# Kernel optimization log

Measured on AMD Instinct MI355X. Metric: run time of the kernel, lower is better.

## Reference

```python
import jax, jax.numpy as jnp
import numpy as np
from jax import lax

CIN, COUT, K_EXP, KSZ = 128, 256, 8, 3
HIDDEN = CIN // 4  # reduction=4
B, H, W = 32, 56, 56
TEMP = 1.0


def setup_inputs() -> dict:
    key = jax.random.key(0)
    ks = jax.random.split(key, 6)
    x = jax.random.normal(ks[0], (B, CIN, H, W), dtype=jnp.float32)
    weight_bank = jax.random.normal(ks[1], (K_EXP, COUT, CIN, KSZ, KSZ), dtype=jnp.float32) * 0.02
    fc1_w = jax.random.normal(ks[2], (HIDDEN, CIN), dtype=jnp.float32) * (1.0 / np.sqrt(CIN))
    fc1_b = jnp.zeros((HIDDEN,), dtype=jnp.float32)
    fc2_w = jax.random.normal(ks[3], (K_EXP, HIDDEN), dtype=jnp.float32) * (1.0 / np.sqrt(HIDDEN))
    fc2_b = jnp.zeros((K_EXP,), dtype=jnp.float32)
    return {"x": x, "weight_bank": weight_bank, "fc1_w": fc1_w, "fc1_b": fc1_b,
            "fc2_w": fc2_w, "fc2_b": fc2_b}


def reference(x, weight_bank, fc1_w, fc1_b, fc2_w, fc2_b):
    b, cin, h, w = x.shape
    # Routing: GAP -> fc1 -> relu -> fc2 -> softmax(/T)
    v = jnp.mean(x, axis=(2, 3))                       # (B, cin)
    hdd = jax.nn.relu(v @ fc1_w.T + fc1_b)             # (B, hidden)
    logits = hdd @ fc2_w.T + fc2_b                     # (B, K)
    a = jax.nn.softmax(logits / TEMP, axis=1)          # (B, K)
    # Per-sample dynamic weights: (B, cout, cin, k, k)
    Wdyn = jnp.einsum('bk,kocij->bocij', a, weight_bank)
    # Batched per-sample conv via grouped convolution:
    # x -> (1, B*cin, H, W), Wdyn -> (B*cout, cin, k, k), groups=B
    xg = x.reshape(1, b * cin, h, w)
    wg = Wdyn.reshape(b * weight_bank.shape[1], cin, KSZ, KSZ)
    y = lax.conv_general_dilated(
        xg, wg,
        window_strides=(1, 1),
        padding=[(1, 1), (1, 1)],
        feature_group_count=b,
        dimension_numbers=('NCHW', 'OIHW', 'NCHW'),
    )
    return y.reshape(b, weight_bank.shape[1], y.shape[2], y.shape[3])
```

## Files before the change

kernel.cpp:

```cpp
#include <hip/hip_runtime.h>


#define CIN    128
#define COUT   256
#define KEXP   8
#define HIDDEN 32
#define B_     32
#define H_     56
#define W_     56
#define HW     3136
#define HP     58
#define WP     58
#define KK     1152

typedef float  v4f  __attribute__((ext_vector_type(4)));
typedef float  v16f __attribute__((ext_vector_type(16)));
typedef __bf16 v8bf __attribute__((ext_vector_type(8)));

__device__ __forceinline__ unsigned short f2bf(float x) {
  unsigned int u = __float_as_uint(x);
  u += 0x7fff + ((u >> 16) & 1);
  return (unsigned short)(u >> 16);
}

__device__ __forceinline__ void gl_lds16(const void* g, void* lds) {
  __builtin_amdgcn_global_load_lds(
      (__attribute__((address_space(1))) void*)(unsigned long long)(g),
      (__attribute__((address_space(3))) void*)(lds),
      16, 0, 0);
}

__global__ __launch_bounds__(256) void k_xpose(const float* __restrict__ x,
                                               unsigned short* __restrict__ xpt,
                                               float* __restrict__ gpart) {
  const int h = blockIdx.x, b = blockIdx.y, tid = threadIdx.x;
  __shared__ __align__(16) unsigned short tfb[56 * 132];
  __shared__ float gp[256];
  const float4* xr4 = (const float4*)x + (size_t)b * CIN * 784;

#pragma unroll
  for (int it = 0; it < 7; ++it) {
    int idx = it * 256 + tid;
    int c  = idx / 14;
    int wq = idx - c * 14;
    float4 q = xr4[(size_t)c * 784 + h * 14 + wq];
    int w0 = wq * 4;
    tfb[(w0 + 0) * 132 + c] = f2bf(q.x);
    tfb[(w0 + 1) * 132 + c] = f2bf(q.y);
    tfb[(w0 + 2) * 132 + c] = f2bf(q.z);
    tfb[(w0 + 3) * 132 + c] = f2bf(q.w);
  }
  __syncthreads();

  {
    int c = tid & 127, half = tid >> 7;
    float s = 0.f;
#pragma unroll
    for (int w = half * 28; w < half * 28 + 28; ++w)
      s += __uint_as_float((unsigned)tfb[w * 132 + c] << 16);
    gp[tid] = s;
  }

#pragma unroll
  for (int it = 0; it < 7; ++it) {
    int idx = it * 256 + tid;
    int w  = idx >> 5;
    int c4 = (idx & 31) << 2;
    ushort4 o = *(const ushort4*)(tfb + w * 132 + c4);
    *(ushort4*)(xpt + ((size_t)(b * HP + (h + 1)) * WP + (w + 1)) * CIN + c4) = o;
  }

  if (tid < 128) {
    size_t rb = (size_t)(b * HP + (h + 1)) * WP * CIN;
    xpt[rb + tid] = 0;
    xpt[rb + 57 * CIN + tid] = 0;
  }
  if (h == 0 || h == 55) {
    int hr = (h == 0) ? 0 : 57;
    size_t rb = (size_t)(b * HP + hr) * WP * CIN;
    ushort4 z; z.x = z.y = z.z = z.w = 0;
    for (int i = tid; i < 1856; i += 256)
      *(ushort4*)(xpt + rb + i * 4) = z;
  }

  __syncthreads();
  if (tid < 128)
    gpart[((size_t)h * B_ + b) * CIN + tid] =
        (gp[tid] + gp[tid + 128]) * (1.0f / 3136.0f);
}

__global__ void k_mlp(const float* __restrict__ gpart, const float* __restrict__ fc1w,
                      const float* __restrict__ fc1b, const float* __restrict__ fc2w,
                      const float* __restrict__ fc2b, float* __restrict__ aout) {
  const int b = blockIdx.x, t = threadIdx.x;
  __shared__ float vS[CIN];
  __shared__ float hid[HIDDEN];
  __shared__ float lg[KEXP];
  {
    float s = 0.f;
    for (int h = 0; h < H_; ++h) s += gpart[((size_t)h * B_ + b) * CIN + t];
    vS[t] = s;
  }
  __syncthreads();
  if (t < HIDDEN) {
    float s = fc1b[t];
    const float* wr = fc1w + t * CIN;
    for (int c = 0; c < CIN; ++c) s += vS[c] * wr[c];
    hid[t] = fmaxf(s, 0.f);
  }
  __syncthreads();
  if (t < KEXP) {
    float s = fc2b[t];
    const float* wr = fc2w + t * HIDDEN;
    for (int j = 0; j < HIDDEN; ++j) s += hid[j] * wr[j];
    lg[t] = s;
  }
  __syncthreads();
  if (t == 0) {
    float m = lg[0];
    for (int k = 1; k < KEXP; ++k) m = fmaxf(m, lg[k]);
    float e[KEXP], den = 0.f;
    for (int k = 0; k < KEXP; ++k) { e[k] = expf(lg[k] - m); den += e[k]; }
    float inv = 1.0f / den;
    for (int k = 0; k < KEXP; ++k) aout[b * KEXP + k] = e[k] * inv;
  }
}

__global__ __launch_bounds__(512) void k_wdyn(const float* __restrict__ aout,
                                              const float* __restrict__ bank,
                                              unsigned short* __restrict__ wdyn) {
  const int cout = blockIdx.x, tid = threadIdx.x;
  __shared__ float4 bS4[KEXP * 288];
  __shared__ float aS[B_ * KEXP];

  for (int idx = tid; idx < KEXP * 288; idx += 512) {
    int k = idx / 288, r = idx - k * 288;
    bS4[idx] = ((const float4*)(bank + (size_t)(k * COUT + cout) * KK))[r];
  }
  if (tid < 256) aS[tid] = aout[tid];
  __syncthreads();

  const float* bS = (const float*)bS4;
  const int lane_kk = tid & 63;
  const int sg = tid >> 6;
  float areg[4][KEXP];
#pragma unroll
  for (int bi = 0; bi < 4; ++bi)
#pragma unroll
    for (int k = 0; k < KEXP; ++k) areg[bi][k] = aS[(sg * 4 + bi) * KEXP + k];

  for (int it = 0; it < 18; ++it) {
    int kk  = it * 64 + lane_kk;
    int khw = kk >> 7, cin = kk & 127;
    int e   = cin * 9 + khw;
    float vv[KEXP];
#pragma unroll
    for (int k = 0; k < KEXP; ++k) vv[k] = bS[k * KK + e];
#pragma unroll
    for (int bi = 0; bi < 4; ++bi) {
      float s = 0.f;
#pragma unroll
      for (int k = 0; k < KEXP; ++k) s += areg[bi][k] * vv[k];
      wdyn[(size_t)((sg * 4 + bi) * COUT + cout) * KK + kk] = f2bf(s);
    }
  }
}

#define BARX()   asm volatile("s_barrier" ::: "memory")
#define WAITV8() asm volatile("s_waitcnt vmcnt(8)" ::: "memory")
#define WAITV0() asm volatile("s_waitcnt vmcnt(0)" ::: "memory")

__device__ __forceinline__ void stage4(const unsigned short* src, unsigned short* dbuf,
                                       const int (&off)[4], int disp, int tid) {
#pragma unroll
  for (int g = 0; g < 4; ++g)
    gl_lds16(src + off[g] + disp, dbuf + (g * 256 + tid) * 8);
}

__device__ __forceinline__ void load4(const unsigned short* base, const int (&pc)[4],
                                      v8bf (&f)[4]) {
#pragma unroll
  for (int ks = 0; ks < 4; ++ks)
    f[ks] = *(const v8bf*)(base + pc[ks]);
}

__device__ __forceinline__ void mfma4(const v8bf (&a)[4], const v8bf (&b)[4], v16f& acc) {
  __builtin_amdgcn_s_setprio(1);
#pragma unroll
  for (int ks = 0; ks < 4; ++ks)
    acc = __builtin_amdgcn_mfma_f32_32x32x16_bf16(a[ks], b[ks], acc, 0, 0, 0);
  __builtin_amdgcn_s_setprio(0);
}

__global__ __launch_bounds__(256, 2) void k_conv128(const unsigned short* __restrict__ wdyn,
                                                    const unsigned short* __restrict__ xpt,
                                                    float* __restrict__ out) {
  extern __shared__ unsigned short sh[];
  unsigned short* A0 = sh;
  unsigned short* A1 = sh + 8192;
  unsigned short* B0 = sh + 16384;
  unsigned short* B1 = sh + 24576;

  const int id  = blockIdx.x;
  const int xcd = id & 7, idx = id >> 3;
  const int bs  = idx / 50;
  const int r   = idx - bs * 50;
  const int b   = xcd * 4 + bs;
  const int bm  = r / 25;
  const int ch  = r - bm * 25;
  const int p0  = ch << 7;

  const int tid = threadIdx.x;
  const int wv = tid >> 6, l = tid & 63;
  const int l31 = l & 31, hi = l >> 5, s7 = l & 7;
  const int wr = wv >> 1, wc = wv & 1;

  const unsigned short* wb = wdyn + ((size_t)b * COUT + bm * 128) * KK;
  const unsigned short* xb = xpt + (size_t)b * HP * WP * CIN;

  int aoff[4], boff[4];
#pragma unroll
  for (int g = 0; g < 4; ++g) {
    int gidx = g * 256 + tid;
    int row = gidx >> 3;
    int c = (gidx & 7) ^ (row & 7);
    aoff[g] = row * KK + c * 8;
    int p = p0 + row;
    p = p > 3135 ? 3135 : p;
    int ph = p / 56, pw = p - ph * 56;
    boff[g] = (ph * WP + pw) * CIN + c * 8;
  }

  const int abase = (wr * 64 + l31) * 64;
  const int bbase = (wc * 64 + l31) * 64;
  int pc[4];
#pragma unroll
  for (int ks = 0; ks < 4; ++ks) pc[ks] = ((2 * ks + hi) ^ s7) * 8;

  v16f acc[2][2];
#pragma unroll
  for (int mi = 0; mi < 2; ++mi)
#pragma unroll
    for (int ni = 0; ni < 2; ++ni)
#pragma unroll
      for (int rr = 0; rr < 16; ++rr) acc[mi][ni][rr] = 0.f;

  stage4(wb, A0, aoff, 0, tid);
  stage4(xb, B0, boff, 0, tid);
  WAITV0();
  BARX();

  v8bf afA[4], bv0[4], bv1[4];

  for (int t = 0; t < 18; ++t) {
    const unsigned short* Ab = (t & 1) ? A1 : A0;
    const unsigned short* Bb = (t & 1) ? B1 : B0;
    unsigned short* An = (t & 1) ? A0 : A1;
    unsigned short* Bn = (t & 1) ? B0 : B1;

    if (t < 17) {
      int tn = t + 1;
      int khw = tn >> 1;
      int kh = (khw * 11) >> 5;
      int kw = khw - 3 * kh;
      stage4(wb, An, aoff, tn * 64, tid);
      stage4(xb, Bn, boff, (kh * WP + kw) * CIN + ((tn & 1) << 6), tid);
      WAITV8();
    } else {
      WAITV0();
    }
    BARX();

    load4(Ab + abase, pc, afA);
    load4(Bb + bbase, pc, bv0);
    mfma4(afA, bv0, acc[0][0]);
    load4(Bb + bbase + 2048, pc, bv1);
    mfma4(afA, bv1, acc[0][1]);
    load4(Ab + abase + 2048, pc, afA);
    mfma4(afA, bv1, acc[1][1]);
    mfma4(afA, bv0, acc[1][0]);
    BARX();
  }

#pragma unroll
  for (int mi = 0; mi < 2; ++mi)
#pragma unroll
    for (int ni = 0; ni < 2; ++ni) {
      int p = p0 + wc * 64 + ni * 32 + l31;
      if (p < HW) {
#pragma unroll
        for (int reg = 0; reg < 16; ++reg) {
          int cout = bm * 128 + wr * 64 + mi * 32 + (reg & 3) + 8 * (reg >> 2) + 4 * hi;
          out[(size_t)(b * COUT + cout) * HW + p] = acc[mi][ni][reg];
        }
      }
    }
}

extern "C" void kernel_launch(void* const* d_in, const int* in_sizes, int n_in,
                              void* d_out, int out_size, void* d_ws, size_t ws_size,
                              hipStream_t stream) {
  const float* x    = (const float*)d_in[0];
  const float* bank = (const float*)d_in[1];
  const float* fc1w = (const float*)d_in[2];
  const float* fc1b = (const float*)d_in[3];
  const float* fc2w = (const float*)d_in[4];
  const float* fc2b = (const float*)d_in[5];
  float* out = (float*)d_out;

  char* ws = (char*)d_ws;
  float* gpart = (float*)(ws + 0);
  float* aout  = (float*)(ws + (1u << 20));
  unsigned short* wdyn = (unsigned short*)(ws + (2u << 20));
  unsigned short* xpt  = (unsigned short*)(ws + (2u << 20) + 18874368);

  static bool attr_done = false;
  if (!attr_done) {
    (void)hipFuncSetAttribute((const void*)k_conv128,
                              hipFuncAttributeMaxDynamicSharedMemorySize, 65536);
    attr_done = true;
  }

  k_xpose<<<dim3(H_, B_), 256, 0, stream>>>(x, xpt, gpart);
  k_mlp<<<dim3(B_), 128, 0, stream>>>(gpart, fc1w, fc1b, fc2w, fc2b, aout);
  k_wdyn<<<dim3(COUT), 512, 0, stream>>>(aout, bank, wdyn);
  k_conv128<<<dim3(1600), 256, 65536, stream>>>(wdyn, xpt, out);
}
```

Baseline: 241.8 us.

## Switch LDS tiles to chunk-major layout and interleave MFMA accumulators

Changes the LDS staging layout from row-major with XOR swizzle to a chunk-major layout, where each 16-byte k-chunk of all 128 rows is stored contiguously, so fragment reads need no swizzle. All A and B fragments are loaded up front and the four accumulator MFMAs are interleaved per k-step instead of run as back-to-back chains. This is meant to cut bank conflicts and swizzle index math and to hide MFMA dependency latency. It raises register pressure from holding four fragment sets and may change the global-to-LDS access coalescing pattern.

```diff
diff --git a/kernel.cpp b/kernel.cpp
--- a/kernel.cpp
+++ b/kernel.cpp
@@ -177,21 +177,6 @@
     gl_lds16(src + off[g] + disp, dbuf + (g * 256 + tid) * 8);
 }
 
-__device__ __forceinline__ void load4(const unsigned short* base, const int (&pc)[4],
-                                      v8bf (&f)[4]) {
-#pragma unroll
-  for (int ks = 0; ks < 4; ++ks)
-    f[ks] = *(const v8bf*)(base + pc[ks]);
-}
-
-__device__ __forceinline__ void mfma4(const v8bf (&a)[4], const v8bf (&b)[4], v16f& acc) {
-  __builtin_amdgcn_s_setprio(1);
-#pragma unroll
-  for (int ks = 0; ks < 4; ++ks)
-    acc = __builtin_amdgcn_mfma_f32_32x32x16_bf16(a[ks], b[ks], acc, 0, 0, 0);
-  __builtin_amdgcn_s_setprio(0);
-}
-
 __global__ __launch_bounds__(256, 2) void k_conv128(const unsigned short* __restrict__ wdyn,
                                                     const unsigned short* __restrict__ xpt,
                                                     float* __restrict__ out) {
@@ -212,30 +197,32 @@
 
   const int tid = threadIdx.x;
   const int wv = tid >> 6, l = tid & 63;
-  const int l31 = l & 31, hi = l >> 5, s7 = l & 7;
+  const int l31 = l & 31, hi = l >> 5;
   const int wr = wv >> 1, wc = wv & 1;
 
   const unsigned short* wb = wdyn + ((size_t)b * COUT + bm * 128) * KK;
   const unsigned short* xb = xpt + (size_t)b * HP * WP * CIN;
 
   int aoff[4], boff[4];
-#pragma unroll
-  for (int g = 0; g < 4; ++g) {
-    int gidx = g * 256 + tid;
-    int row = gidx >> 3;
-    int c = (gidx & 7) ^ (row & 7);
-    aoff[g] = row * KK + c * 8;
+  {
+    int row = tid & 127;
     int p = p0 + row;
     p = p > 3135 ? 3135 : p;
     int ph = p / 56, pw = p - ph * 56;
-    boff[g] = (ph * WP + pw) * CIN + c * 8;
-  }
-
-  const int abase = (wr * 64 + l31) * 64;
-  const int bbase = (wc * 64 + l31) * 64;
+    int prow = (ph * WP + pw) * CIN;
+#pragma unroll
+    for (int g = 0; g < 4; ++g) {
+      int chunk = g * 2 + (tid >> 7);
+      aoff[g] = row * KK + chunk * 8;
+      boff[g] = prow + chunk * 8;
+    }
+  }
+
+  const int arow = (wr * 64 + l31) * 8;
+  const int brow = (wc * 64 + l31) * 8;
   int pc[4];
 #pragma unroll
-  for (int ks = 0; ks < 4; ++ks) pc[ks] = ((2 * ks + hi) ^ s7) * 8;
+  for (int ks = 0; ks < 4; ++ks) pc[ks] = (2 * ks + hi) * 1024;
 
   v16f acc[2][2];
 #pragma unroll
@@ -249,8 +236,6 @@
   stage4(xb, B0, boff, 0, tid);
   WAITV0();
   BARX();
-
-  v8bf afA[4], bv0[4], bv1[4];
 
   for (int t = 0; t < 18; ++t) {
     const unsigned short* Ab = (t & 1) ? A1 : A0;
@@ -271,14 +256,26 @@
     }
     BARX();
 
-    load4(Ab + abase, pc, afA);
-    load4(Bb + bbase, pc, bv0);
-    mfma4(afA, bv0, acc[0][0]);
-    load4(Bb + bbase + 2048, pc, bv1);
-    mfma4(afA, bv1, acc[0][1]);
-    load4(Ab + abase + 2048, pc, afA);
-    mfma4(afA, bv1, acc[1][1]);
-    mfma4(afA, bv0, acc[1][0]);
+    v8bf afA[4], afB[4], bv0[4], bv1[4];
+#pragma unroll
+    for (int ks = 0; ks < 4; ++ks) {
+      afA[ks] = *(const v8bf*)(Ab + pc[ks] + arow);
+      bv0[ks] = *(const v8bf*)(Bb + pc[ks] + brow);
+    }
+#pragma unroll
+    for (int ks = 0; ks < 4; ++ks) {
+      bv1[ks] = *(const v8bf*)(Bb + pc[ks] + brow + 256);
+      afB[ks] = *(const v8bf*)(Ab + pc[ks] + arow + 256);
+    }
+    __builtin_amdgcn_s_setprio(1);
+#pragma unroll
+    for (int ks = 0; ks < 4; ++ks) {
+      acc[0][0] = __builtin_amdgcn_mfma_f32_32x32x16_bf16(afA[ks], bv0[ks], acc[0][0], 0, 0, 0);
+      acc[0][1] = __builtin_amdgcn_mfma_f32_32x32x16_bf16(afA[ks], bv1[ks], acc[0][1], 0, 0, 0);
+      acc[1][0] = __builtin_amdgcn_mfma_f32_32x32x16_bf16(afB[ks], bv0[ks], acc[1][0], 0, 0, 0);
+      acc[1][1] = __builtin_amdgcn_mfma_f32_32x32x16_bf16(afB[ks], bv1[ks], acc[1][1], 0, 0, 0);
+    }
+    __builtin_amdgcn_s_setprio(0);
     BARX();
   }
 
```

Result: slower. 280.8 us (+16.1%).
